# Kernel optimization log

Measured on AMD Instinct MI355X. Metric: run time of the kernel, lower is better.

The kernel has to match this reference:

```python
import jax, jax.numpy as jnp
import numpy as np

N_HEAD = 16
HEAD_DIM = 64
ROPE_BASE = 10000.0


def _rope_cos_sin(T, dim, dtype):
    inv_freq = 1.0 / (ROPE_BASE ** (np.arange(0, dim, 2, dtype=np.float32) / dim))
    t = np.arange(T, dtype=np.float32)
    freqs = np.outer(t, inv_freq)              # [T, dim/2]
    emb = np.concatenate([freqs, freqs], -1)   # [T, dim]
    return jnp.asarray(np.cos(emb), dtype), jnp.asarray(np.sin(emb), dtype)


def _rotate_half(x):
    x1, x2 = x[..., : x.shape[-1] // 2], x[..., x.shape[-1] // 2 :]
    return jnp.concatenate([-x2, x1], axis=-1)


def setup_inputs() -> dict:
    key = jax.random.key(0)
    k1, k2, k3 = jax.random.split(key, 3)
    B, T, C = 4, 2048, 1024
    x = jax.random.normal(k1, (B, T, C), jnp.float32)
    w_qkv = jax.random.normal(k2, (C, 3 * C), jnp.float32) * (C ** -0.5)
    w_proj = jax.random.normal(k3, (C, C), jnp.float32) * (C ** -0.5)
    return {"x": x, "w_qkv": w_qkv, "w_proj": w_proj}


def reference(x, w_qkv, w_proj):
    B, T, C = x.shape
    H, D = N_HEAD, HEAD_DIM
    qkv = x @ w_qkv                                   # [B, T, 3C]
    q, k, v = jnp.split(qkv, 3, axis=-1)
    # [B, H, T, D]
    q = q.reshape(B, T, H, D).transpose(0, 2, 1, 3)
    k = k.reshape(B, T, H, D).transpose(0, 2, 1, 3)
    v = v.reshape(B, T, H, D).transpose(0, 2, 1, 3)
    cos, sin = _rope_cos_sin(T, D, x.dtype)           # [T, D]
    q = q * cos + _rotate_half(q) * sin
    k = k * cos + _rotate_half(k) * sin
    scale = D ** -0.5
    scores = jnp.einsum("bhqd,bhkd->bhqk", q, k) * scale
    causal = jnp.tril(jnp.ones((T, T), bool))
    scores = jnp.where(causal, scores, jnp.finfo(scores.dtype).min)
    attn = jax.nn.softmax(scores, axis=-1)
    y = jnp.einsum("bhqk,bhkd->bhqd", attn, v)        # [B, H, T, D]
    y = y.transpose(0, 2, 1, 3).reshape(B, T, C)
    return y @ w_proj
```

## Files before the change

kernel.cpp:

```cpp
#include <hip/hip_runtime.h>
#include <cstdint>

typedef unsigned short u16;
typedef __attribute__((ext_vector_type(4))) float f32x4;
typedef __attribute__((ext_vector_type(4))) unsigned short u16x4;
typedef __attribute__((ext_vector_type(8))) unsigned short u16x8;
typedef __attribute__((ext_vector_type(8))) __bf16 bf16x8;

#define DEV __device__ __forceinline__

DEV u16 f2bf(float f) {
  union { float f; uint32_t u; } x{f};
  uint32_t r = (x.u + 0x7fffu + ((x.u >> 16) & 1u)) >> 16;
  return (u16)r;
}

DEV void gl_lds16(const void* g, void* l) {
  __builtin_amdgcn_global_load_lds((__attribute__((address_space(1))) void*)(g),
                                   (__attribute__((address_space(3))) void*)(l),
                                   16, 0, 0);
}

__global__ __launch_bounds__(256) void cast_f2b(const float* __restrict__ in,
                                                u16* __restrict__ out) {
  int i = blockIdx.x * 256 + threadIdx.x;
  float4 v = ((const float4*)in)[i];
  u16x4 o = { f2bf(v.x), f2bf(v.y), f2bf(v.z), f2bf(v.w) };
  ((u16x4*)out)[i] = o;
}

__global__ __launch_bounds__(256) void transpose_cast(const float* __restrict__ in,
                                                      u16* __restrict__ out, int R, int C) {
  __shared__ float tile[64][65];
  const int c0 = blockIdx.x * 64, r0 = blockIdx.y * 64;
  const int tx = threadIdx.x & 63, ty = threadIdx.x >> 6;
  for (int r = ty; r < 64; r += 4) tile[r][tx] = in[(size_t)(r0 + r) * C + c0 + tx];
  __syncthreads();
  for (int r = ty; r < 64; r += 4) out[(size_t)(c0 + r) * R + r0 + tx] = f2bf(tile[tx][r]);
}

template <int EPI>
__global__ __launch_bounds__(256) void gemm_bt(const u16* __restrict__ A,
                                               const u16* __restrict__ Bt,
                                               u16* __restrict__ qo, u16* __restrict__ ko,
                                               u16* __restrict__ vo, float* __restrict__ outf) {
  const int K = 1024;
  __shared__ __align__(16) u16 As[128 * 32];
  __shared__ __align__(16) u16 Bs[128 * 32];
  const int m0 = blockIdx.y * 128, n0 = blockIdx.x * 128;
  const int tid = threadIdx.x;
  const int w = tid >> 6, lane = tid & 63, quad = lane >> 4, l15 = lane & 15;
  const int mw = (w >> 1) * 64, nw = (w & 1) * 64;
  const int srow = lane >> 2, scol = (lane & 3) * 8;

  f32x4 acc[4][4];
#pragma unroll
  for (int i = 0; i < 4; ++i)
#pragma unroll
    for (int j = 0; j < 4; ++j) acc[i][j] = f32x4{0.f, 0.f, 0.f, 0.f};

  const u16* ga0 = A + (size_t)(m0 + srow) * K + scol;
  const u16* gb0 = Bt + (size_t)(n0 + srow) * K + scol;

  for (int k0 = 0; k0 < K; k0 += 32) {
#pragma unroll
    for (int cc = 0; cc < 2; ++cc) {
      int c = w + cc * 4;
      gl_lds16(ga0 + (size_t)c * 16 * K + k0, As + c * 512 + lane * 8);
      gl_lds16(gb0 + (size_t)c * 16 * K + k0, Bs + c * 512 + lane * 8);
    }
    __syncthreads();
    bf16x8 af[4], bfv[4];
#pragma unroll
    for (int i = 0; i < 4; ++i)
      af[i] = *(const bf16x8*)(As + (mw + i * 16 + l15) * 32 + quad * 8);
#pragma unroll
    for (int j = 0; j < 4; ++j)
      bfv[j] = *(const bf16x8*)(Bs + (nw + j * 16 + l15) * 32 + quad * 8);
#pragma unroll
    for (int i = 0; i < 4; ++i)
#pragma unroll
      for (int j = 0; j < 4; ++j)
        acc[i][j] = __builtin_amdgcn_mfma_f32_16x16x32_bf16(af[i], bfv[j], acc[i][j], 0, 0, 0);
    __syncthreads();
  }

  if (EPI == 1) {
#pragma unroll
    for (int i = 0; i < 4; ++i)
#pragma unroll
      for (int j = 0; j < 4; ++j)
#pragma unroll
        for (int r = 0; r < 4; ++r) {
          int row = m0 + mw + i * 16 + quad * 4 + r;
          int col = n0 + nw + j * 16 + l15;
          outf[(size_t)row * 1024 + col] = acc[i][j][r];
        }
    return;
  }
  const int s = n0 >> 10;
  const int hh = ((n0 & 1023) + nw) >> 6;
  if (s == 2) {
#pragma unroll
    for (int i = 0; i < 4; ++i)
#pragma unroll
      for (int r = 0; r < 4; ++r) {
        int row = m0 + mw + i * 16 + quad * 4 + r;
        int b = row >> 11, t = row & 2047;
        size_t base = ((size_t)(b * 16 + hh) * 2048 + t) * 64;
#pragma unroll
        for (int j = 0; j < 4; ++j) vo[base + j * 16 + l15] = f2bf(acc[i][j][r]);
      }
  } else {
    u16* dst = (s == 0) ? qo : ko;
    const float QS = (s == 0) ? 0.18033688011112042f : 1.0f;
    const float C1 = -0.4152410118609203f;
    const float R2PI = 0.15915494309189535f;
    const float inv0 = __builtin_amdgcn_exp2f((float)l15 * C1) * R2PI;
    const float inv1 = __builtin_amdgcn_exp2f((float)(16 + l15) * C1) * R2PI;
#pragma unroll
    for (int i = 0; i < 4; ++i)
#pragma unroll
      for (int r = 0; r < 4; ++r) {
        int row = m0 + mw + i * 16 + quad * 4 + r;
        int b = row >> 11, t = row & 2047;
        size_t base = ((size_t)(b * 16 + hh) * 2048 + t) * 64;
        float tf = (float)t;
        float a0 = tf * inv0; a0 -= floorf(a0);
        float a1 = tf * inv1; a1 -= floorf(a1);
        float c0 = __builtin_amdgcn_cosf(a0), s0 = __builtin_amdgcn_sinf(a0);
        float c1 = __builtin_amdgcn_cosf(a1), s1 = __builtin_amdgcn_sinf(a1);
        float x0 = acc[i][0][r], y0 = acc[i][2][r];
        float x1 = acc[i][1][r], y1 = acc[i][3][r];
        dst[base + l15]      = f2bf((x0 * c0 - y0 * s0) * QS);
        dst[base + 32 + l15] = f2bf((y0 * c0 + x0 * s0) * QS);
        dst[base + 16 + l15] = f2bf((x1 * c1 - y1 * s1) * QS);
        dst[base + 48 + l15] = f2bf((y1 * c1 + x1 * s1) * QS);
      }
  }
}

__global__ __launch_bounds__(256) void transpose_v(const u16* __restrict__ v,
                                                   u16* __restrict__ vt) {
  const int bh = blockIdx.y, t0 = blockIdx.x * 64;
  __shared__ __align__(16) u16 tile[64][72];
  const int tid = threadIdx.x;
  const int row = tid >> 3, col = (tid & 7) * 8;
#pragma unroll
  for (int rr = 0; rr < 2; ++rr) {
    int r = row + rr * 32;
    *(u16x8*)(&tile[r][col]) = *(const u16x8*)(v + ((size_t)bh * 2048 + t0 + r) * 64 + col);
  }
  __syncthreads();
#pragma unroll
  for (int rr = 0; rr < 2; ++rr) {
    int d = row + rr * 32;
    u16x8 o;
#pragma unroll
    for (int j = 0; j < 8; ++j) o[j] = tile[col + j][d];
    *(u16x8*)(vt + ((size_t)bh * 64 + d) * 2048 + t0 + col) = o;
  }
}

__global__ __launch_bounds__(256) void attn_kernel(const u16* __restrict__ q,
                                                   const u16* __restrict__ k,
                                                   const u16* __restrict__ vt,
                                                   u16* __restrict__ y) {
  const int T = 2048;
  const int bh = blockIdx.x;
  const int qi = 15 - blockIdx.y;
  const int q0 = qi * 128;
  const int tid = threadIdx.x;
  const int w = tid >> 6, lane = tid & 63, quad = lane >> 4, l15 = lane & 15;
  __shared__ __align__(16) u16 Ks[64 * 64];
  __shared__ __align__(16) u16 Vs[64 * 64];
  __shared__ __align__(16) u16 Pq[4 * 32 * 72];
  u16* Pw = Pq + w * 32 * 72;

  const int sw = l15 & 7;
  int koff[4][2], voff[4][2];
#pragma unroll
  for (int kf = 0; kf < 4; ++kf) {
    koff[kf][0] = (kf * 16 + l15) * 64 + ((quad ^ sw) * 8);
    koff[kf][1] = (kf * 16 + l15) * 64 + (((quad + 4) ^ sw) * 8);
  }
#pragma unroll
  for (int df = 0; df < 4; ++df) {
    voff[df][0] = (df * 16 + l15) * 64 + ((quad ^ sw) * 8);
    voff[df][1] = (df * 16 + l15) * 64 + (((quad + 4) ^ sw) * 8);
  }
  const int pwoff = l15 * 72 + quad * 4;
  const int proff = l15 * 72 + quad * 8;

  const int r_ = tid >> 3, c_ = tid & 7, ssw = r_ & 7;
  const u16* kg = k + (size_t)bh * T * 64;
  const u16* vg = vt + (size_t)bh * 64 * T;
  const int sk0 = r_ * 64 + (c_ ^ ssw) * 8;
  const int sk1 = (r_ + 32) * 64 + (c_ ^ ssw) * 8;
  const int sv0 = r_ * T + (c_ ^ ssw) * 8;
  const int sv1 = (r_ + 32) * T + (c_ ^ ssw) * 8;

  const int b_ = bh >> 4, h_ = bh & 15;
  const int q0w = q0 + w * 32;

  bf16x8 qf_[2][2];
#pragma unroll
  for (int qf = 0; qf < 2; ++qf)
#pragma unroll
    for (int h = 0; h < 2; ++h)
      qf_[qf][h] = *(const bf16x8*)(q + ((size_t)bh * T + q0w + qf * 16 + l15) * 64 + h * 32 + quad * 8);

  f32x4 o[2][4];
  float li[2] = {0.f, 0.f};
#pragma unroll
  for (int qf = 0; qf < 2; ++qf)
#pragma unroll
    for (int df = 0; df < 4; ++df) o[qf][df] = f32x4{0.f, 0.f, 0.f, 0.f};

  const int nit = 2 * qi + 2;

  for (int it = 0; it < nit; ++it) {
    const int kb = it * 64;
    gl_lds16(kg + (size_t)kb * 64 + sk0, Ks + tid * 8);
    gl_lds16(kg + (size_t)kb * 64 + sk1, Ks + 2048 + tid * 8);
    gl_lds16(vg + kb + sv0, Vs + tid * 8);
    gl_lds16(vg + kb + sv1, Vs + 2048 + tid * 8);
    __syncthreads();

    bf16x8 ka[4][2];
#pragma unroll
    for (int kf = 0; kf < 4; ++kf) {
      ka[kf][0] = *(const bf16x8*)(Ks + koff[kf][0]);
      ka[kf][1] = *(const bf16x8*)(Ks + koff[kf][1]);
    }
    f32x4 st[2][4];
#pragma unroll
    for (int kf = 0; kf < 4; ++kf)
#pragma unroll
      for (int qf = 0; qf < 2; ++qf) {
        f32x4 s = f32x4{0.f, 0.f, 0.f, 0.f};
        s = __builtin_amdgcn_mfma_f32_16x16x32_bf16(ka[kf][0], qf_[qf][0], s, 0, 0, 0);
        s = __builtin_amdgcn_mfma_f32_16x16x32_bf16(ka[kf][1], qf_[qf][1], s, 0, 0, 0);
        st[qf][kf] = s;
      }

    if (it >= nit - 2) {
#pragma unroll
      for (int qf = 0; qf < 2; ++qf) {
        const int qrow = q0w + qf * 16 + l15;
#pragma unroll
        for (int kf = 0; kf < 4; ++kf)
#pragma unroll
          for (int r = 0; r < 4; ++r)
            if (kb + kf * 16 + quad * 4 + r > qrow) st[qf][kf][r] = -__builtin_inff();
      }
    }

#pragma unroll
    for (int qf = 0; qf < 2; ++qf) {
      float rs = 0.f;
#pragma unroll
      for (int kf = 0; kf < 4; ++kf) {
        float p0 = __builtin_amdgcn_exp2f(st[qf][kf][0]);
        float p1 = __builtin_amdgcn_exp2f(st[qf][kf][1]);
        float p2 = __builtin_amdgcn_exp2f(st[qf][kf][2]);
        float p3 = __builtin_amdgcn_exp2f(st[qf][kf][3]);
        rs += (p0 + p1) + (p2 + p3);
        union { float f; uint32_t u; } u0{p0}, u1{p1}, u2{p2}, u3{p3};
        uint32_t pk01 = __builtin_amdgcn_perm(u1.u + 0x8000u, u0.u + 0x8000u, 0x07060302u);
        uint32_t pk23 = __builtin_amdgcn_perm(u3.u + 0x8000u, u2.u + 0x8000u, 0x07060302u);
        uint2 pk; pk.x = pk01; pk.y = pk23;
        *(uint2*)(Pw + qf * 16 * 72 + pwoff + kf * 16) = pk;
      }
      li[qf] += rs;
    }

#pragma unroll
    for (int qf = 0; qf < 2; ++qf) {
      bf16x8 pb0 = *(const bf16x8*)(Pw + qf * 16 * 72 + proff);
      bf16x8 pb1 = *(const bf16x8*)(Pw + qf * 16 * 72 + proff + 32);
#pragma unroll
      for (int df = 0; df < 4; ++df) {
        bf16x8 va0 = *(const bf16x8*)(Vs + voff[df][0]);
        bf16x8 va1 = *(const bf16x8*)(Vs + voff[df][1]);
        o[qf][df] = __builtin_amdgcn_mfma_f32_16x16x32_bf16(va0, pb0, o[qf][df], 0, 0, 0);
        o[qf][df] = __builtin_amdgcn_mfma_f32_16x16x32_bf16(va1, pb1, o[qf][df], 0, 0, 0);
      }
    }
    __syncthreads();
  }

#pragma unroll
  for (int qf = 0; qf < 2; ++qf) {
    float l = li[qf];
    l += __shfl_xor(l, 16, 64);
    l += __shfl_xor(l, 32, 64);
    const float inv = 1.f / l;
    const size_t base = ((size_t)b_ * 2048 + q0w + qf * 16 + l15) * 1024 + h_ * 64;
#pragma unroll
    for (int df = 0; df < 4; ++df) {
      u16x4 ov;
#pragma unroll
      for (int r = 0; r < 4; ++r) ov[r] = f2bf(o[qf][df][r] * inv);
      *(u16x4*)(y + base + df * 16 + quad * 4) = ov;
    }
  }
}

extern "C" void kernel_launch(void* const* d_in, const int* in_sizes, int n_in,
                              void* d_out, int out_size, void* d_ws, size_t ws_size,
                              hipStream_t stream) {
  const float* x = (const float*)d_in[0];
  const float* w_qkv = (const float*)d_in[1];
  const float* w_proj = (const float*)d_in[2];
  float* out = (float*)d_out;

  u16* xb = (u16*)d_ws;
  u16* wqkvT = xb + 8388608;
  u16* wprojT = wqkvT + 3145728;
  u16* qb = wprojT + 1048576;
  u16* kbuf = qb + 8388608;
  u16* vb = kbuf + 8388608;
  u16* vtb = vb + 8388608;
  u16* yb = xb;

  cast_f2b<<<8192, 256, 0, stream>>>(x, xb);
  transpose_cast<<<dim3(48, 16), 256, 0, stream>>>(w_qkv, wqkvT, 1024, 3072);
  transpose_cast<<<dim3(16, 16), 256, 0, stream>>>(w_proj, wprojT, 1024, 1024);
  gemm_bt<0><<<dim3(24, 64), 256, 0, stream>>>(xb, wqkvT, qb, kbuf, vb, nullptr);
  transpose_v<<<dim3(32, 64), 256, 0, stream>>>(vb, vtb);
  attn_kernel<<<dim3(64, 16), 256, 0, stream>>>(qb, kbuf, vtb, yb);
  gemm_bt<1><<<dim3(8, 64), 256, 0, stream>>>(yb, wprojT, nullptr, nullptr, nullptr, out);
}
```

Baseline: 263.6 us.

## Double GEMM K-tile to 64 and XOR-swizzle LDS layout to avoid bank conflicts

The bf16 GEMM now stages a K-slice of 64 per iteration instead of 32, which halves the number of barrier pairs and load rounds per tile. The LDS layout gets an XOR swizzle on the 16-byte chunk index, so fragment reads from rows 128 bytes apart spread across banks instead of conflicting. LDS use per block doubles to 32 KB, which may reduce occupancy. There is still no double buffering, so loads and MFMAs do not overlap.

```diff
diff --git a/kernel.cpp b/kernel.cpp
--- a/kernel.cpp
+++ b/kernel.cpp
@@ -45,13 +45,15 @@
                                                u16* __restrict__ qo, u16* __restrict__ ko,
                                                u16* __restrict__ vo, float* __restrict__ outf) {
   const int K = 1024;
-  __shared__ __align__(16) u16 As[128 * 32];
-  __shared__ __align__(16) u16 Bs[128 * 32];
+  __shared__ __align__(16) u16 As[128 * 64];
+  __shared__ __align__(16) u16 Bs[128 * 64];
   const int m0 = blockIdx.y * 128, n0 = blockIdx.x * 128;
   const int tid = threadIdx.x;
   const int w = tid >> 6, lane = tid & 63, quad = lane >> 4, l15 = lane & 15;
   const int mw = (w >> 1) * 64, nw = (w & 1) * 64;
-  const int srow = lane >> 2, scol = (lane & 3) * 8;
+
+  const int srow = tid >> 3;
+  const int schunk = ((tid & 7) ^ (srow & 7)) * 8;
 
   f32x4 acc[4][4];
 #pragma unroll
@@ -59,29 +61,39 @@
 #pragma unroll
     for (int j = 0; j < 4; ++j) acc[i][j] = f32x4{0.f, 0.f, 0.f, 0.f};
 
-  const u16* ga0 = A + (size_t)(m0 + srow) * K + scol;
-  const u16* gb0 = Bt + (size_t)(n0 + srow) * K + scol;
-
-  for (int k0 = 0; k0 < K; k0 += 32) {
-#pragma unroll
-    for (int cc = 0; cc < 2; ++cc) {
-      int c = w + cc * 4;
-      gl_lds16(ga0 + (size_t)c * 16 * K + k0, As + c * 512 + lane * 8);
-      gl_lds16(gb0 + (size_t)c * 16 * K + k0, Bs + c * 512 + lane * 8);
+  const u16* ga0 = A + (size_t)(m0 + srow) * K + schunk;
+  const u16* gb0 = Bt + (size_t)(n0 + srow) * K + schunk;
+
+  const int sw7 = l15 & 7;
+  int aoff[4], boff[4];
+#pragma unroll
+  for (int i = 0; i < 4; ++i) aoff[i] = (mw + i * 16 + l15) * 64;
+#pragma unroll
+  for (int j = 0; j < 4; ++j) boff[j] = (nw + j * 16 + l15) * 64;
+  int coff[2];
+#pragma unroll
+  for (int kk = 0; kk < 2; ++kk) coff[kk] = ((kk * 4 + quad) ^ sw7) * 8;
+
+  for (int k0 = 0; k0 < K; k0 += 64) {
+#pragma unroll
+    for (int ss = 0; ss < 4; ++ss) {
+      gl_lds16(ga0 + (size_t)ss * 32 * K + k0, As + ss * 2048 + tid * 8);
+      gl_lds16(gb0 + (size_t)ss * 32 * K + k0, Bs + ss * 2048 + tid * 8);
     }
     __syncthreads();
-    bf16x8 af[4], bfv[4];
-#pragma unroll
-    for (int i = 0; i < 4; ++i)
-      af[i] = *(const bf16x8*)(As + (mw + i * 16 + l15) * 32 + quad * 8);
-#pragma unroll
-    for (int j = 0; j < 4; ++j)
-      bfv[j] = *(const bf16x8*)(Bs + (nw + j * 16 + l15) * 32 + quad * 8);
-#pragma unroll
-    for (int i = 0; i < 4; ++i)
-#pragma unroll
-      for (int j = 0; j < 4; ++j)
-        acc[i][j] = __builtin_amdgcn_mfma_f32_16x16x32_bf16(af[i], bfv[j], acc[i][j], 0, 0, 0);
+#pragma unroll
+    for (int kk = 0; kk < 2; ++kk) {
+      bf16x8 af[4], bfv[4];
+#pragma unroll
+      for (int i = 0; i < 4; ++i) af[i] = *(const bf16x8*)(As + aoff[i] + coff[kk]);
+#pragma unroll
+      for (int j = 0; j < 4; ++j) bfv[j] = *(const bf16x8*)(Bs + boff[j] + coff[kk]);
+#pragma unroll
+      for (int i = 0; i < 4; ++i)
+#pragma unroll
+        for (int j = 0; j < 4; ++j)
+          acc[i][j] = __builtin_amdgcn_mfma_f32_16x16x32_bf16(af[i], bfv[j], acc[i][j], 0, 0, 0);
+    }
     __syncthreads();
   }
 
```

Result: faster. 248.5 us (-5.7%).
